# Kernel tuning notes

Hardware: AMD Instinct MI355X
Metric: run time of the kernel (lower is better)

The kernel has to match this reference:

```python
import jax, jax.numpy as jnp
import numpy as np

SEQ_LEN = 4096
D_IN = 1024
D_OUT = 1024


def setup_inputs() -> dict:
    key = jax.random.key(0)
    k_x, k_q, k_k, k_v = jax.random.split(key, 4)
    s = 1.0 / np.sqrt(D_IN)
    return {
        "x": jax.random.normal(k_x, (SEQ_LEN, D_IN), dtype=jnp.float32),
        "W_query": jax.random.normal(k_q, (D_IN, D_OUT), dtype=jnp.float32) * s,
        "W_key": jax.random.normal(k_k, (D_IN, D_OUT), dtype=jnp.float32) * s,
        "W_value": jax.random.normal(k_v, (D_IN, D_OUT), dtype=jnp.float32) * s,
    }


def reference(x, W_query, W_key, W_value):
    # QKV projections (Linear without bias): [S, d_out]
    q = x @ W_query
    k = x @ W_key
    v = x @ W_value
    # Full S x S score matrix, causal mask, scaled softmax
    scores = q @ k.T  # [S, S]
    seq_len = x.shape[0]
    causal = jnp.tril(jnp.ones((seq_len, seq_len), dtype=bool))
    scores = jnp.where(causal, scores, -jnp.inf)
    scale = 1.0 / jnp.sqrt(jnp.asarray(k.shape[-1], dtype=scores.dtype))
    attn = jax.nn.softmax(scores * scale, axis=-1)
    return attn @ v  # [S, d_out]
```

## Files before the change

kernel.cpp:

```cpp
#include <hip/hip_runtime.h>
#include <math.h>

#define SEQ 4096
#define DIM 1024

typedef unsigned short u16;
typedef __attribute__((ext_vector_type(8))) short short8;
typedef __attribute__((ext_vector_type(4))) float floatx4;
typedef __attribute__((ext_vector_type(4))) unsigned short us4;

__device__ __forceinline__ float bf2f(u16 u) {
    union { unsigned int i; float f; } c; c.i = ((unsigned int)u) << 16; return c.f;
}
__device__ __forceinline__ u16 f2bf(float f) {
    union { float f; unsigned int i; } c; c.f = f;
    return (u16)((c.i + 0x7fffu + ((c.i >> 16) & 1u)) >> 16);
}
__device__ __forceinline__ void gload_lds16(const u16* g, u16* l) {
    __builtin_amdgcn_global_load_lds((const __attribute__((address_space(1))) void*)g,
                                     (__attribute__((address_space(3))) void*)l, 16, 0, 0);
}

template <int MODE>
__global__ __launch_bounds__(256) void gemm_nt(const u16* __restrict__ A,
                                               const u16* __restrict__ B,
                                               void* __restrict__ Cv,
                                               float* __restrict__ Ppart,
                                               u16* __restrict__ VtOut,
                                               int lda, int ldb, int ldc, int Kdim,
                                               float scale0) {
    const int row0 = blockIdx.y * 128;
    const int col0 = blockIdx.x * 128;
    if (MODE == 1 && col0 > row0) return;
    int kbeg = 0, kend = Kdim, chunk = 0;
    if (MODE == 2) {
        chunk = blockIdx.z;
        kbeg = chunk << 10;
        const int klim = row0 + 128;
        if (kbeg >= klim) return;
        kend = min(kbeg + 1024, klim);
    }

    __shared__ u16 As[3][4096];
    __shared__ u16 Bs[3][4096];

    const int tid  = threadIdx.x;
    const int wave = tid >> 6;
    const int lane = tid & 63;
    const int wm = wave & 1;
    const int wn = wave >> 1;

    const int s0 = wave * 128 + lane;
    const int s1 = s0 + 64;
    const int r0s = s0 >> 2, q0s = ((s0 & 3) ^ ((s0 >> 3) & 3)) * 8;
    const int r1s = s1 >> 2, q1s = ((s1 & 3) ^ ((s1 >> 3) & 3)) * 8;
    const u16* aP0 = A + (size_t)(row0 + r0s) * lda + kbeg + q0s;
    const u16* aP1 = A + (size_t)(row0 + r1s) * lda + kbeg + q1s;
    const u16* bP0 = B + (size_t)(col0 + r0s) * ldb + kbeg + q0s;
    const u16* bP1 = B + (size_t)(col0 + r1s) * ldb + kbeg + q1s;
    const int l0 = wave * 1024;

    floatx4 acc[4][4] = {};
    const int niter = (kend - kbeg) >> 5;
    const int frow = lane & 15;
    const int xq = (((lane >> 4) ^ ((frow >> 1) & 3))) * 8;

    gload_lds16(aP0, &As[0][l0]);
    gload_lds16(aP1, &As[0][l0 + 512]);
    gload_lds16(bP0, &Bs[0][l0]);
    gload_lds16(bP1, &Bs[0][l0 + 512]);
    aP0 += 32; aP1 += 32; bP0 += 32; bP1 += 32;
    gload_lds16(aP0, &As[1][l0]);
    gload_lds16(aP1, &As[1][l0 + 512]);
    gload_lds16(bP0, &Bs[1][l0]);
    gload_lds16(bP1, &Bs[1][l0 + 512]);
    aP0 += 32; aP1 += 32; bP0 += 32; bP1 += 32;

    auto compute_tile = [&](int c) {
        short8 af[4], bfr[4];
#pragma unroll
        for (int t = 0; t < 4; ++t) {
            af[t]  = *(const short8*)&As[c][(wm * 64 + t * 16 + frow) * 32 + xq];
            bfr[t] = *(const short8*)&Bs[c][(wn * 64 + t * 16 + frow) * 32 + xq];
        }
#pragma unroll
        for (int mt = 0; mt < 4; ++mt)
#pragma unroll
            for (int nt = 0; nt < 4; ++nt)
                acc[mt][nt] = __builtin_amdgcn_mfma_f32_16x16x32_bf16(
                    af[mt], bfr[nt], acc[mt][nt], 0, 0, 0);
    };

    int cur = 0, pre = 2;
    for (int it = 0; it < niter - 2; ++it) {
        asm volatile("s_waitcnt vmcnt(4)\n\ts_barrier" ::: "memory");
        {
            short8 af[4], bfr[4];
#pragma unroll
            for (int t = 0; t < 4; ++t) {
                af[t]  = *(const short8*)&As[cur][(wm * 64 + t * 16 + frow) * 32 + xq];
                bfr[t] = *(const short8*)&Bs[cur][(wn * 64 + t * 16 + frow) * 32 + xq];
            }
            gload_lds16(aP0, &As[pre][l0]);
            gload_lds16(aP1, &As[pre][l0 + 512]);
            gload_lds16(bP0, &Bs[pre][l0]);
            gload_lds16(bP1, &Bs[pre][l0 + 512]);
            aP0 += 32; aP1 += 32; bP0 += 32; bP1 += 32;
#pragma unroll
            for (int mt = 0; mt < 4; ++mt)
#pragma unroll
                for (int nt = 0; nt < 4; ++nt)
                    acc[mt][nt] = __builtin_amdgcn_mfma_f32_16x16x32_bf16(
                        af[mt], bfr[nt], acc[mt][nt], 0, 0, 0);
        }
        cur = (cur == 2) ? 0 : cur + 1;
        pre = (pre == 2) ? 0 : pre + 1;
    }
    asm volatile("s_waitcnt vmcnt(4)\n\ts_barrier" ::: "memory");
    compute_tile(cur);
    cur = (cur == 2) ? 0 : cur + 1;
    asm volatile("s_waitcnt vmcnt(0)\n\ts_barrier" ::: "memory");
    compute_tile(cur);

    const int cr = (lane >> 4) * 4;
    const int cc = lane & 15;
    if (MODE == 2) {
        float* dst;
        if (chunk == 0) {
            dst = (float*)Cv;
        } else {
            const ptrdiff_t poff[3] = {0, (ptrdiff_t)3072 * 1024, (ptrdiff_t)5120 * 1024};
            dst = Ppart + poff[chunk - 1] - (ptrdiff_t)(chunk << 10) * 1024;
        }
#pragma unroll
        for (int mt = 0; mt < 4; ++mt)
#pragma unroll
            for (int nt = 0; nt < 4; ++nt)
#pragma unroll
                for (int r = 0; r < 4; ++r) {
                    const int row = row0 + wm * 64 + mt * 16 + cr + r;
                    const int col = col0 + wn * 64 + nt * 16 + cc;
                    dst[(size_t)row * ldc + col] = acc[mt][nt][r];
                }
    } else if (MODE == 0 && col0 >= 2048) {
#pragma unroll
        for (int mt = 0; mt < 4; ++mt)
#pragma unroll
            for (int nt = 0; nt < 4; ++nt) {
                const int row = row0 + wm * 64 + mt * 16 + cr;
                const int col = (col0 - 2048) + wn * 64 + nt * 16 + cc;
                us4 o = { f2bf(acc[mt][nt][0]), f2bf(acc[mt][nt][1]),
                          f2bf(acc[mt][nt][2]), f2bf(acc[mt][nt][3]) };
                *(us4*)&VtOut[(size_t)col * SEQ + row] = o;
            }
    } else {
        u16* dst = (u16*)Cv;
        const float sc = (MODE == 0 && col0 < 1024) ? scale0 : 1.0f;
#pragma unroll
        for (int mt = 0; mt < 4; ++mt)
#pragma unroll
            for (int nt = 0; nt < 4; ++nt)
#pragma unroll
                for (int r = 0; r < 4; ++r) {
                    const int row = row0 + wm * 64 + mt * 16 + cr + r;
                    const int col = col0 + wn * 64 + nt * 16 + cc;
                    dst[(size_t)row * ldc + col] = f2bf(acc[mt][nt][r] * sc);
                }
    }
}

__global__ __launch_bounds__(256) void transpose_cast(const float* __restrict__ W0,
                                                      const float* __restrict__ W1,
                                                      const float* __restrict__ W2,
                                                      u16* __restrict__ Wt) {
    __shared__ float tile[32][33];
    const float* W = (blockIdx.z == 0) ? W0 : (blockIdx.z == 1) ? W1 : W2;
    u16* out = Wt + (size_t)blockIdx.z * DIM * DIM;
    const int bx = blockIdx.x * 32;
    const int by = blockIdx.y * 32;
    const int tx = threadIdx.x & 31;
    const int ty = (threadIdx.x >> 5) * 4;
#pragma unroll
    for (int r = 0; r < 4; ++r)
        tile[ty + r][tx] = W[(size_t)(by + ty + r) * DIM + bx + tx];
    __syncthreads();
#pragma unroll
    for (int r = 0; r < 4; ++r)
        out[(size_t)(bx + ty + r) * DIM + by + tx] = f2bf(tile[tx][ty + r]);
}

__global__ __launch_bounds__(256) void cast_bf16(const float* __restrict__ X,
                                                 u16* __restrict__ Xb) {
    const size_t i = ((size_t)blockIdx.x * 256 + threadIdx.x) * 4;
    const float4 v = *(const float4*)(X + i);
    us4 o = { f2bf(v.x), f2bf(v.y), f2bf(v.z), f2bf(v.w) };
    *(us4*)(Xb + i) = o;
}

__global__ __launch_bounds__(256) void softmax_causal_bf16(u16* __restrict__ S) {
    __shared__ float red[4];
    __shared__ float bc;
    const int i = blockIdx.x;
    u16* row = S + (size_t)i * SEQ;
    const int n = i + 1;
    const int tid = threadIdx.x;
    const int zend = (i & ~127) + 128;

    float v[16];
    float m = -3.4e38f;
#pragma unroll
    for (int t = 0; t < 16; ++t) {
        const int j = tid + (t << 8);
        if (j < n) { v[t] = bf2f(row[j]); m = fmaxf(m, v[t]); }
    }
#pragma unroll
    for (int o = 32; o > 0; o >>= 1) m = fmaxf(m, __shfl_down(m, o));
    if ((tid & 63) == 0) red[tid >> 6] = m;
    __syncthreads();
    if (tid == 0) bc = fmaxf(fmaxf(red[0], red[1]), fmaxf(red[2], red[3]));
    __syncthreads();
    m = bc;

    float s = 0.f;
#pragma unroll
    for (int t = 0; t < 16; ++t) {
        const int j = tid + (t << 8);
        if (j < n) { v[t] = __expf(v[t] - m); s += v[t]; }
    }
#pragma unroll
    for (int o = 32; o > 0; o >>= 1) s += __shfl_down(s, o);
    if ((tid & 63) == 0) red[tid >> 6] = s;
    __syncthreads();
    if (tid == 0) bc = 1.0f / (red[0] + red[1] + red[2] + red[3]);
    __syncthreads();
    const float inv = bc;

#pragma unroll
    for (int t = 0; t < 16; ++t) {
        const int j = tid + (t << 8);
        if (j < n) row[j] = f2bf(v[t] * inv);
        else if (j < zend) row[j] = 0;
    }
}

__global__ __launch_bounds__(256) void reduce_pv(float* __restrict__ O,
                                                 const float* __restrict__ P) {
    const int r = blockIdx.x;
    const int row = 1024 + r;
    const int col = threadIdx.x * 4;
    float4 a = *(const float4*)(O + (size_t)row * 1024 + col);
    const float4 b1 = *(const float4*)(P + (size_t)r * 1024 + col);
    a.x += b1.x; a.y += b1.y; a.z += b1.z; a.w += b1.w;
    if (row >= 2048) {
        const float4 b2 = *(const float4*)(P + (size_t)3072 * 1024 +
                                           (size_t)(row - 2048) * 1024 + col);
        a.x += b2.x; a.y += b2.y; a.z += b2.z; a.w += b2.w;
    }
    if (row >= 3072) {
        const float4 b3 = *(const float4*)(P + (size_t)5120 * 1024 +
                                           (size_t)(row - 3072) * 1024 + col);
        a.x += b3.x; a.y += b3.y; a.z += b3.z; a.w += b3.w;
    }
    *(float4*)(O + (size_t)row * 1024 + col) = a;
}

extern "C" void kernel_launch(void* const* d_in, const int* in_sizes, int n_in,
                              void* d_out, int out_size, void* d_ws, size_t ws_size,
                              hipStream_t stream) {
    const float* x  = (const float*)d_in[0];
    const float* Wq = (const float*)d_in[1];
    const float* Wk = (const float*)d_in[2];
    const float* Wv = (const float*)d_in[3];

    u16* xb    = (u16*)d_ws;
    u16* Wt    = xb  + (size_t)SEQ * DIM;
    u16* QK    = Wt  + (size_t)3072 * DIM;
    u16* Vt    = QK  + (size_t)SEQ * 2048;
    u16* S     = Vt  + (size_t)DIM * SEQ;
    float* Ppart = (float*)(S + (size_t)SEQ * SEQ);

    cast_bf16<<<SEQ * DIM / 1024, 256, 0, stream>>>(x, xb);
    transpose_cast<<<dim3(32, 32, 3), 256, 0, stream>>>(Wq, Wk, Wv, Wt);

    gemm_nt<0><<<dim3(24, 32), 256, 0, stream>>>(
        xb, Wt, QK, nullptr, Vt, DIM, DIM, 2048, DIM, 0.03125f);

    gemm_nt<1><<<dim3(32, 32), 256, 0, stream>>>(
        QK, QK + 1024, S, nullptr, nullptr, 2048, 2048, SEQ, DIM, 1.0f);

    softmax_causal_bf16<<<SEQ, 256, 0, stream>>>(S);

    gemm_nt<2><<<dim3(8, 32, 4), 256, 0, stream>>>(
        S, Vt, d_out, Ppart, nullptr, SEQ, SEQ, DIM, SEQ, 1.0f);

    reduce_pv<<<3072, 256, 0, stream>>>((float*)d_out, Ppart);
}
```

Before: 211.1 us.

## Fuse causal softmax exponent into QK GEMM epilogue and defer normalization

```diff
diff --git a/kernel.cpp b/kernel.cpp
--- a/kernel.cpp
+++ b/kernel.cpp
@@ -27,6 +27,7 @@
                                                void* __restrict__ Cv,
                                                float* __restrict__ Ppart,
                                                u16* __restrict__ VtOut,
+                                               float* __restrict__ Lsum,
                                                int lda, int ldb, int ldc, int Kdim,
                                                float scale0) {
     const int row0 = blockIdx.y * 128;
@@ -94,25 +95,23 @@
     int cur = 0, pre = 2;
     for (int it = 0; it < niter - 2; ++it) {
         asm volatile("s_waitcnt vmcnt(4)\n\ts_barrier" ::: "memory");
-        {
-            short8 af[4], bfr[4];
-#pragma unroll
-            for (int t = 0; t < 4; ++t) {
-                af[t]  = *(const short8*)&As[cur][(wm * 64 + t * 16 + frow) * 32 + xq];
-                bfr[t] = *(const short8*)&Bs[cur][(wn * 64 + t * 16 + frow) * 32 + xq];
-            }
-            gload_lds16(aP0, &As[pre][l0]);
-            gload_lds16(aP1, &As[pre][l0 + 512]);
-            gload_lds16(bP0, &Bs[pre][l0]);
-            gload_lds16(bP1, &Bs[pre][l0 + 512]);
-            aP0 += 32; aP1 += 32; bP0 += 32; bP1 += 32;
-#pragma unroll
-            for (int mt = 0; mt < 4; ++mt)
-#pragma unroll
-                for (int nt = 0; nt < 4; ++nt)
-                    acc[mt][nt] = __builtin_amdgcn_mfma_f32_16x16x32_bf16(
-                        af[mt], bfr[nt], acc[mt][nt], 0, 0, 0);
-        }
+        short8 af[4], bfr[4];
+#pragma unroll
+        for (int t = 0; t < 4; ++t) {
+            af[t]  = *(const short8*)&As[cur][(wm * 64 + t * 16 + frow) * 32 + xq];
+            bfr[t] = *(const short8*)&Bs[cur][(wn * 64 + t * 16 + frow) * 32 + xq];
+        }
+        gload_lds16(aP0, &As[pre][l0]);
+        gload_lds16(aP1, &As[pre][l0 + 512]);
+        gload_lds16(bP0, &Bs[pre][l0]);
+        gload_lds16(bP1, &Bs[pre][l0 + 512]);
+        aP0 += 32; aP1 += 32; bP0 += 32; bP1 += 32;
+#pragma unroll
+        for (int mt = 0; mt < 4; ++mt)
+#pragma unroll
+            for (int nt = 0; nt < 4; ++nt)
+                acc[mt][nt] = __builtin_amdgcn_mfma_f32_16x16x32_bf16(
+                    af[mt], bfr[nt], acc[mt][nt], 0, 0, 0);
         cur = (cur == 2) ? 0 : cur + 1;
         pre = (pre == 2) ? 0 : pre + 1;
     }
@@ -124,7 +123,29 @@
 
     const int cr = (lane >> 4) * 4;
     const int cc = lane & 15;
-    if (MODE == 2) {
+    if (MODE == 1) {
+        u16* dst = (u16*)Cv;
+#pragma unroll
+        for (int mt = 0; mt < 4; ++mt) {
+#pragma unroll
+            for (int r = 0; r < 4; ++r) {
+                const int grow = row0 + wm * 64 + mt * 16 + cr + r;
+                float rowsum = 0.f;
+#pragma unroll
+                for (int nt = 0; nt < 4; ++nt) {
+                    const int gcol = col0 + wn * 64 + nt * 16 + cc;
+                    const float e = (gcol <= grow) ? __expf(acc[mt][nt][r]) : 0.f;
+                    rowsum += e;
+                    dst[(size_t)grow * ldc + gcol] = f2bf(e);
+                }
+                rowsum += __shfl_xor(rowsum, 1);
+                rowsum += __shfl_xor(rowsum, 2);
+                rowsum += __shfl_xor(rowsum, 4);
+                rowsum += __shfl_xor(rowsum, 8);
+                if (cc == 0) atomicAdd(&Lsum[grow], rowsum);
+            }
+        }
+    } else if (MODE == 2) {
         float* dst;
         if (chunk == 0) {
             dst = (float*)Cv;
@@ -135,13 +156,15 @@
 #pragma unroll
         for (int mt = 0; mt < 4; ++mt)
 #pragma unroll
-            for (int nt = 0; nt < 4; ++nt)
-#pragma unroll
-                for (int r = 0; r < 4; ++r) {
-                    const int row = row0 + wm * 64 + mt * 16 + cr + r;
+            for (int r = 0; r < 4; ++r) {
+                const int grow = row0 + wm * 64 + mt * 16 + cr + r;
+                const float invl = 1.0f / Lsum[grow];
+#pragma unroll
+                for (int nt = 0; nt < 4; ++nt) {
                     const int col = col0 + wn * 64 + nt * 16 + cc;
-                    dst[(size_t)row * ldc + col] = acc[mt][nt][r];
+                    dst[(size_t)grow * ldc + col] = acc[mt][nt][r] * invl;
                 }
+            }
     } else if (MODE == 0 && col0 >= 2048) {
 #pragma unroll
         for (int mt = 0; mt < 4; ++mt)
@@ -155,7 +178,7 @@
             }
     } else {
         u16* dst = (u16*)Cv;
-        const float sc = (MODE == 0 && col0 < 1024) ? scale0 : 1.0f;
+        const float sc = (col0 < 1024) ? scale0 : 1.0f;
 #pragma unroll
         for (int mt = 0; mt < 4; ++mt)
 #pragma unroll
@@ -190,57 +213,13 @@
 }
 
 __global__ __launch_bounds__(256) void cast_bf16(const float* __restrict__ X,
-                                                 u16* __restrict__ Xb) {
+                                                 u16* __restrict__ Xb,
+                                                 float* __restrict__ Lsum) {
+    if (blockIdx.x < 16) Lsum[blockIdx.x * 256 + threadIdx.x] = 0.f;
     const size_t i = ((size_t)blockIdx.x * 256 + threadIdx.x) * 4;
     const float4 v = *(const float4*)(X + i);
     us4 o = { f2bf(v.x), f2bf(v.y), f2bf(v.z), f2bf(v.w) };
     *(us4*)(Xb + i) = o;
-}
-
-__global__ __launch_bounds__(256) void softmax_causal_bf16(u16* __restrict__ S) {
-    __shared__ float red[4];
-    __shared__ float bc;
-    const int i = blockIdx.x;
-    u16* row = S + (size_t)i * SEQ;
-    const int n = i + 1;
-    const int tid = threadIdx.x;
-    const int zend = (i & ~127) + 128;
-
-    float v[16];
-    float m = -3.4e38f;
-#pragma unroll
-    for (int t = 0; t < 16; ++t) {
-        const int j = tid + (t << 8);
-        if (j < n) { v[t] = bf2f(row[j]); m = fmaxf(m, v[t]); }
-    }
-#pragma unroll
-    for (int o = 32; o > 0; o >>= 1) m = fmaxf(m, __shfl_down(m, o));
-    if ((tid & 63) == 0) red[tid >> 6] = m;
-    __syncthreads();
-    if (tid == 0) bc = fmaxf(fmaxf(red[0], red[1]), fmaxf(red[2], red[3]));
-    __syncthreads();
-    m = bc;
-
-    float s = 0.f;
-#pragma unroll
-    for (int t = 0; t < 16; ++t) {
-        const int j = tid + (t << 8);
-        if (j < n) { v[t] = __expf(v[t] - m); s += v[t]; }
-    }
-#pragma unroll
-    for (int o = 32; o > 0; o >>= 1) s += __shfl_down(s, o);
-    if ((tid & 63) == 0) red[tid >> 6] = s;
-    __syncthreads();
-    if (tid == 0) bc = 1.0f / (red[0] + red[1] + red[2] + red[3]);
-    __syncthreads();
-    const float inv = bc;
-
-#pragma unroll
-    for (int t = 0; t < 16; ++t) {
-        const int j = tid + (t << 8);
-        if (j < n) row[j] = f2bf(v[t] * inv);
-        else if (j < zend) row[j] = 0;
-    }
 }
 
 __global__ __launch_bounds__(256) void reduce_pv(float* __restrict__ O,
@@ -276,22 +255,21 @@
     u16* Wt    = xb  + (size_t)SEQ * DIM;
     u16* QK    = Wt  + (size_t)3072 * DIM;
     u16* Vt    = QK  + (size_t)SEQ * 2048;
-    u16* S     = Vt  + (size_t)DIM * SEQ;
-    float* Ppart = (float*)(S + (size_t)SEQ * SEQ);
-
-    cast_bf16<<<SEQ * DIM / 1024, 256, 0, stream>>>(x, xb);
+    u16* E     = Vt  + (size_t)DIM * SEQ;
+    float* Ppart = (float*)(E + (size_t)SEQ * SEQ);
+    float* Lsum  = Ppart + (size_t)8192 * 1024;
+
+    cast_bf16<<<SEQ * DIM / 1024, 256, 0, stream>>>(x, xb, Lsum);
     transpose_cast<<<dim3(32, 32, 3), 256, 0, stream>>>(Wq, Wk, Wv, Wt);
 
     gemm_nt<0><<<dim3(24, 32), 256, 0, stream>>>(
-        xb, Wt, QK, nullptr, Vt, DIM, DIM, 2048, DIM, 0.03125f);
+        xb, Wt, QK, nullptr, Vt, nullptr, DIM, DIM, 2048, DIM, 0.03125f);
 
     gemm_nt<1><<<dim3(32, 32), 256, 0, stream>>>(
-        QK, QK + 1024, S, nullptr, nullptr, 2048, 2048, SEQ, DIM, 1.0f);
-
-    softmax_causal_bf16<<<SEQ, 256, 0, stream>>>(S);
+        QK, QK + 1024, E, nullptr, nullptr, Lsum, 2048, 2048, SEQ, DIM, 1.0f);
 
     gemm_nt<2><<<dim3(8, 32, 4), 256, 0, stream>>>(
-        S, Vt, d_out, Ppart, nullptr, SEQ, SEQ, DIM, SEQ, 1.0f);
+        E, Vt, d_out, Ppart, nullptr, Lsum, SEQ, SEQ, DIM, SEQ, 1.0f);
 
     reduce_pv<<<3072, 256, 0, stream>>>((float*)d_out, Ppart);
 }
```

After: 201.9 us. 4.4% less time.
